# Kernel optimization log

Hardware: AMD Instinct MI355X
Metric: run time of the kernel (lower is better)

## Reference

```python
import jax, jax.numpy as jnp
import numpy as np
from jax import lax

WL = 140      # window_length
OFC = 118     # ofc_channel = window_length - 21 - 1
TDN = 21      # TimeDelayNum (sliding time-delay count)
D_CM = 16     # cm_attn embed dim
N_BR = 4      # conv_eeg_audio_number
C_OUT = 10    # conv_output_channel
KS = 9        # conv kernel size

def _init(key, shape, fan_in):
    return jax.random.uniform(key, shape, jnp.float32, -1.0, 1.0) / np.sqrt(fan_in)

def setup_inputs():
    key = jax.random.key(0)
    ks = jax.random.split(key, 12)
    return {
        "x": jax.random.normal(ks[0], (1, 1, 18, WL), dtype=jnp.float32),
        "tdA_in_w": _init(ks[1], (3 * OFC, OFC), OFC),
        "tdA_in_b": jnp.zeros((3 * OFC,), jnp.float32),
        "tdA_out_w": _init(ks[2], (OFC, OFC), OFC),
        "tdA_out_b": jnp.zeros((OFC,), jnp.float32),
        "tdB_in_w": _init(ks[3], (3 * OFC, OFC), OFC),
        "tdB_in_b": jnp.zeros((3 * OFC,), jnp.float32),
        "tdB_out_w": _init(ks[4], (OFC, OFC), OFC),
        "tdB_out_b": jnp.zeros((OFC,), jnp.float32),
        "cm_in_w": _init(ks[5], (N_BR, 3 * D_CM, D_CM), D_CM),
        "cm_in_b": jnp.zeros((N_BR, 3 * D_CM), jnp.float32),
        "cm_out_w": _init(ks[6], (N_BR, D_CM, D_CM), D_CM),
        "cm_out_b": jnp.zeros((N_BR, D_CM), jnp.float32),
        "projA_w": _init(ks[7], (16, 1), 1),
        "projB_w": _init(ks[8], (16, 1), 1),
        "conv_w": _init(ks[9], (N_BR, C_OUT, 16, KS), 16 * KS),
        "conv_b": jnp.zeros((N_BR, C_OUT), jnp.float32),
        "fc1_w": _init(ks[10], (40, 40), 40),
        "fc1_b": jnp.zeros((40,), jnp.float32),
        "fc2_w": _init(ks[11], (2, 40), 40),
        "fc2_b": jnp.zeros((2,), jnp.float32),
    }

def _mha(q, k, v, in_w, in_b, out_w, out_b):
    # single-head attention; q: (Lq, d), k/v: (Lk, d) -> (Lq, d)
    d = q.shape[-1]
    wq, wk, wv = jnp.split(in_w, 3, axis=0)
    bq, bk, bv = jnp.split(in_b, 3)
    qp = (q @ wq.T + bq) * (1.0 / np.sqrt(d))
    kp = k @ wk.T + bk
    vp = v @ wv.T + bv
    attn = jax.nn.softmax(qp @ kp.T, axis=-1)
    return (attn @ vp) @ out_w.T + out_b

def _forward(x, tdA_in_w, tdA_in_b, tdA_out_w, tdA_out_b,
             tdB_in_w, tdB_in_b, tdB_out_w, tdB_out_b,
             cm_in_w, cm_in_b, cm_out_w, cm_out_b,
             projA_w, projB_w, conv_w, conv_b,
             fc1_w, fc1_b, fc2_w, fc2_b):
    sig = x[0, 0]                               # (18, 140)
    wavA_raw, eeg_raw, wavB_raw = sig[0], sig[1:17], sig[17]
    # ChannelWav: sliding time-delay unfold -> (TDN, OFC)
    idx = jnp.arange(TDN)[:, None] + jnp.arange(OFC)[None, :]
    kA = wavA_raw[idx]                          # (21, 118)
    kB = wavB_raw[idx]
    eeg = eeg_raw[:, WL - OFC:]                 # (16, 118)
    # time-delay attention (embed_dim = 118, seq = 16 eeg channels / 21 delays)
    attA = _mha(eeg, kA, kA, tdA_in_w, tdA_in_b, tdA_out_w, tdA_out_b)  # (16, 118)
    attB = _mha(eeg, kB, kB, tdB_in_w, tdB_in_b, tdB_out_w, tdB_out_b)
    # select_max: pick attention row with largest total correlation to eeg
    iA = jnp.argmax(jnp.sum(eeg @ attA.T, axis=1))
    iB = jnp.argmax(jnp.sum(eeg @ attB.T, axis=1))
    wA = projA_w @ attA[iA][None, :]            # 1x1 conv == outer product, (16, 118)
    wB = projB_w @ attB[iB][None, :]
    data = [wA, eeg, eeg, wB]
    kv = [eeg, wA, wB, eeg]
    feats = []
    for i in range(N_BR):                       # 4 structurally distinct branches
        o = _mha(data[i].T, kv[i].T, kv[i].T,
                 cm_in_w[i], cm_in_b[i], cm_out_w[i], cm_out_b[i])      # (118, 16)
        y = lax.conv_general_dilated(o.T[None], conv_w[i], (1,), 'VALID')  # (1, 10, 110)
        y = jax.nn.relu(y[0] + conv_b[i][:, None])
        feats.append(jnp.max(y, axis=-1))       # AdaptiveMaxPool1d(1) -> (10,)
    flat = jnp.concatenate(feats)               # (40,)
    h = jax.nn.sigmoid(flat @ fc1_w.T + fc1_b)
    out = jax.nn.sigmoid(h @ fc2_w.T + fc2_b)
    return out[None, :]                         # (1, 2)

def reference(x, tdA_in_w, tdA_in_b, tdA_out_w, tdA_out_b,
              tdB_in_w, tdB_in_b, tdB_out_w, tdB_out_b,
              cm_in_w, cm_in_b, cm_out_w, cm_out_b,
              projA_w, projB_w, conv_w, conv_b,
              fc1_w, fc1_b, fc2_w, fc2_b):
    return _forward(x, tdA_in_w, tdA_in_b, tdA_out_w, tdA_out_b,
                    tdB_in_w, tdB_in_b, tdB_out_w, tdB_out_b,
                    cm_in_w, cm_in_b, cm_out_w, cm_out_b,
                    projA_w, projB_w, conv_w, conv_b,
                    fc1_w, fc1_b, fc2_w, fc2_b)
```

## Files before the change

kernel.cpp:

```cpp
#include <hip/hip_runtime.h>
#include <math.h>

#define WL   140
#define OFC  118
#define TDN  21
#define COUT 10
#define KS   9
#define IW_SZ (OFC * OFC)

#define PROJ_STRIDE 6848
#define KP_OFF      1888
#define VP_OFF      4368
#define WS_ATT_A    13696
#define WS_ATT_B    13824
#define WS_FEATS    13952
#define WS_FLAGS    14080

#define MAGIC 0x1F2E3D4C
#define NSLOTS 34

struct Params {
    const float *x;
    const float *tdA_in_w, *tdA_in_b, *tdA_out_w, *tdA_out_b;
    const float *tdB_in_w, *tdB_in_b, *tdB_out_w, *tdB_out_b;
    const float *cm_in_w, *cm_in_b, *cm_out_w, *cm_out_b;
    const float *projA_w, *projB_w, *conv_w, *conv_b;
    const float *fc1_w, *fc1_b, *fc2_w, *fc2_b;
    float *fc_unused;
    float *ws, *out;
};

struct TdSm {
    float owpad[OFC][122];
    float qpp[16][122];
    float kpp[TDN][122];
    float vpp[TDN][122];
    float attn[16][22];
    float acs[22];
    float avcs[120];
    float colsum[120];
    float Ssum[16];
    float avsel[120];
    int   sel;
};

struct BrSm {
    float arow[120];
    float pv[16];
    float eeg_s[16][OFC];
    float w_inT[16][48];
    float b_in[48];
    float tv[3][16];
    float w_out[16][16];
    float b_out[16];
    float cw[COUT * 16 * KS];
    float cb[COUT];
    float kpS[OFC][17];
    float vpS[OFC][17];
    float u[120], v2[120];
    float part_m[4][128];
    float part_l[4][128];
    float part_acc[4][OFC][17];
    float o2[OFC][17];
    float qpS[OFC][17];
    float a_[120], dvec[120];
    float Avec[16], Bvec[16];
    float Gc[COUT][KS], cb2[COUT];
    float y[COUT][22];
};

struct HdSm { float f[64]; float h[64]; };

union alignas(16) Sm { TdSm t; BrSm b; HdSm h; };

__device__ inline float wred(float v) {
    #pragma unroll
    for (int off = 32; off; off >>= 1) v += __shfl_xor(v, off);
    return v;
}

__device__ inline void postM(int* f, int tid) {
    __syncthreads();
    if (tid == 0)
        __hip_atomic_store(f, MAGIC, __ATOMIC_RELEASE, __HIP_MEMORY_SCOPE_AGENT);
}

__device__ inline void waitM(int* base, int first, int n, int tid) {
    if (tid == 0) {
        for (int i = 0; i < n; ++i) {
            int* f = base + (first + i) * 16;
            while (__hip_atomic_load(f, __ATOMIC_RELAXED, __HIP_MEMORY_SCOPE_AGENT) != MAGIC)
                __builtin_amdgcn_s_sleep(1);
        }
        __builtin_amdgcn_fence(__ATOMIC_ACQUIRE, "agent");
    }
    __syncthreads();
}

__device__ void td_proj_direct(int side, int lw, int lane, const Params& p)
{
    int sec, o, r, R;
    if (lw < 30) {
        sec = 0; o = lw * 4 + (lane & 3); r = lane >> 2; R = 16;
    } else {
        sec = (lw < 70) ? 1 : 2;
        int base = (lw - (sec == 1 ? 30 : 70)) * 3;
        o = base + lane % 3; r = lane / 3; R = TDN;
    }
    if (o >= OFC || r >= R) return;

    const float* in_w = (side ? p.tdB_in_w : p.tdA_in_w) + sec * IW_SZ + o * OFC;
    const float  bias = (side ? p.tdB_in_b : p.tdA_in_b)[sec * OFC + o];
    const float2* w2  = (const float2*)in_w;
    float s0 = 0.f;

    if (sec == 0) {
        const float2* a = (const float2*)(p.x + (1 + r) * WL + (WL - OFC));
        #pragma unroll 4
        for (int j = 0; j < 59; ++j) {
            float2 u = a[j], w = w2[j];
            s0 += u.x * w.x + u.y * w.y;
        }
        s0 = (s0 + bias) * (1.0f / sqrtf(118.0f));
    } else {
        const float* wr = p.x + (side ? 17 * WL : 0) + r;
        #pragma unroll 4
        for (int j = 0; j < 59; ++j) {
            float2 w = w2[j];
            s0 += wr[2 * j] * w.x + wr[2 * j + 1] * w.y;
        }
        s0 += bias;
    }
    p.ws[side * PROJ_STRIDE
         + (sec == 0 ? 0 : (sec == 1 ? KP_OFF : VP_OFF))
         + r * OFC + o] = s0;
}

__device__ void td_phase2(int b, int tid, const Params& p, TdSm& s)
{
    const float* base  = p.ws + b * PROJ_STRIDE;
    const float* out_b = b ? p.tdB_out_b : p.tdA_out_b;
    const int wid = tid >> 6, lane = tid & 63;

    for (int e = tid; e < 16 * 59; e += 512) {
        int r = e / 59, j = e - r * 59;
        ((float2*)&s.qpp[r][0])[j] = ((const float2*)(base + r * OFC))[j];
    }
    for (int e = tid; e < TDN * 59; e += 512) {
        int t = e / 59, j = e - t * 59;
        ((float2*)&s.kpp[t][0])[j] = ((const float2*)(base + KP_OFF + t * OFC))[j];
        ((float2*)&s.vpp[t][0])[j] = ((const float2*)(base + VP_OFF + t * OFC))[j];
    }
    __syncthreads();

    if (tid < 16 * TDN) {
        int i = tid / TDN, t = tid - (tid / TDN) * TDN;
        const float2* q = (const float2*)&s.qpp[i][0];
        const float2* k = (const float2*)&s.kpp[t][0];
        float sc = 0.f;
        #pragma unroll 4
        for (int j = 0; j < 59; ++j) {
            float2 u = q[j], v = k[j];
            sc += u.x * v.x + u.y * v.y;
        }
        s.attn[i][t] = sc;
    }
    __syncthreads();

    if (tid < 16) {
        float m = s.attn[tid][0];
        for (int t = 1; t < TDN; ++t) m = fmaxf(m, s.attn[tid][t]);
        float l = 0.f;
        for (int t = 0; t < TDN; ++t) {
            float pp = __expf(s.attn[tid][t] - m);
            s.attn[tid][t] = pp;
            l += pp;
        }
        float inv = 1.f / l;
        for (int t = 0; t < TDN; ++t) s.attn[tid][t] *= inv;
    }
    __syncthreads();

    if (tid < TDN) {
        float a = 0.f;
        for (int i = 0; i < 16; ++i) a += s.attn[i][tid];
        s.acs[tid] = a;
    }
    __syncthreads();

    if (tid < OFC) {
        float a = 0.f;
        for (int t = 0; t < TDN; ++t) a += s.acs[t] * s.vpp[t][tid];
        s.avcs[tid] = a;
    }
    __syncthreads();

    if (tid < OFC) {
        const float2* a  = (const float2*)&s.avcs[0];
        const float2* w2 = (const float2*)&s.owpad[tid][0];
        float a0 = 0.f;
        #pragma unroll 4
        for (int j = 0; j < 59; ++j) {
            float2 u = a[j], v = w2[j];
            a0 += u.x * v.x + u.y * v.y;
        }
        s.colsum[tid] = a0 + 16.f * out_b[tid];
    }
    __syncthreads();

    for (int d = wid; d < 16; d += 8) {
        const float* er = p.x + (1 + d) * WL + (WL - OFC);
        int j0 = lane * 2;
        float sc = 0.f;
        if (j0 < OFC) {
            float2 ev = *(const float2*)(er + j0);
            float2 cv = *(const float2*)(&s.colsum[j0]);
            sc = ev.x * cv.x + ev.y * cv.y;
        }
        sc = wred(sc);
        if (lane == 0) s.Ssum[d] = sc;
    }
    __syncthreads();

    if (tid == 0) {
        int best = 0; float bv = s.Ssum[0];
        for (int i = 1; i < 16; ++i)
            if (s.Ssum[i] > bv) { bv = s.Ssum[i]; best = i; }
        s.sel = best;
    }
    __syncthreads();

    if (tid < OFC) {
        float a = 0.f;
        for (int t = 0; t < TDN; ++t) a += s.attn[s.sel][t] * s.vpp[t][tid];
        s.avsel[tid] = a;
    }
    __syncthreads();

    if (tid < OFC) {
        const float2* a  = (const float2*)&s.avsel[0];
        const float2* w2 = (const float2*)&s.owpad[tid][0];
        float a0 = 0.f;
        #pragma unroll 4
        for (int j = 0; j < 59; ++j) {
            float2 u = a[j], v = w2[j];
            a0 += u.x * v.x + u.y * v.y;
        }
        p.ws[(b ? WS_ATT_B : WS_ATT_A) + tid] = a0 + out_b[tid];
    }
}

__device__ void br_pre(int br, int tid, const Params& p, BrSm& s)
{
    const bool d_r1 = (br == 0 || br == 3);

    for (int e = tid; e < 16 * OFC; e += 512) {
        int r = e / OFC, c = e - (e / OFC) * OFC;
        s.eeg_s[r][c] = p.x[(1 + r) * WL + (WL - OFC) + c];
    }
    for (int e = tid; e < 768; e += 512) {
        int q = e / 16, r = e % 16;
        s.w_inT[r][q] = p.cm_in_w[br * 768 + e];
    }
    if (tid < 48) s.b_in[tid] = p.cm_in_b[br * 48 + tid];
    if (tid >= 64 && tid < 320) {
        int e = tid - 64;
        s.w_out[e >> 4][e & 15] = p.cm_out_w[br * 256 + e];
    }
    if (tid >= 384 && tid < 400) s.b_out[tid - 384] = p.cm_out_b[br * 16 + (tid - 384)];
    for (int e = tid; e < COUT * 16 * KS; e += 512) s.cw[e] = p.conv_w[br * 1440 + e];
    if (tid >= 400 && tid < 410) s.cb[tid - 400] = p.conv_b[br * COUT + (tid - 400)];
    {
        const float* pvg = (br < 2) ? p.projA_w : p.projB_w;
        if (tid >= 416 && tid < 432) s.pv[tid - 416] = pvg[tid - 416];
    }
    __syncthreads();

    if (tid < 48) {
        float a = 0.f;
        #pragma unroll
        for (int r = 0; r < 16; ++r) a += s.pv[r] * s.w_inT[r][tid];
        s.tv[tid / 16][tid % 16] = a;
    }
    __syncthreads();

    if (d_r1) {
        for (int e = tid; e < 2 * OFC * 16; e += 512) {
            int sec01 = e / (OFC * 16);
            int rem = e - sec01 * OFC * 16;
            int j = rem >> 4, o = rem & 15;
            float a = 0.f;
            #pragma unroll
            for (int r = 0; r < 16; ++r) a += s.eeg_s[r][j] * s.w_inT[r][(1 + sec01) * 16 + o];
            a += s.b_in[(1 + sec01) * 16 + o];
            (sec01 ? &s.vpS[0][0] : &s.kpS[0][0])[j * 17 + o] = a;
        }
        __syncthreads();
        if (tid < OFC) {
            float uu = 0.f, vv = 0.f;
            #pragma unroll
            for (int o = 0; o < 16; ++o) {
                float kv = s.kpS[tid][o];
                uu += s.tv[0][o] * kv;
                vv += s.b_in[o] * kv;
            }
            s.u[tid] = uu; s.v2[tid] = vv;
        }
    } else {
        for (int e = tid; e < OFC * 16; e += 512) {
            int j = e >> 4, o = e & 15;
            float a = 0.f;
            #pragma unroll
            for (int r = 0; r < 16; ++r) a += s.eeg_s[r][j] * s.w_inT[r][o];
            s.qpS[j][o] = (a + s.b_in[o]) * 0.25f;
        }
        __syncthreads();
        if (tid < OFC) {
            float a = 0.f;
            #pragma unroll
            for (int o = 0; o < 16; ++o) a += s.qpS[tid][o] * s.tv[1][o];
            s.a_[tid] = a;
        }
        if (tid >= 128 && tid < 144) {
            int c = tid - 128;
            float A = 0.f, B = 0.f;
            #pragma unroll
            for (int o = 0; o < 16; ++o) {
                A += s.tv[2][o] * s.w_out[c][o];
                B += s.b_in[32 + o] * s.w_out[c][o];
            }
            s.Avec[c] = A;
            s.Bvec[c] = B + s.b_out[c];
        }
        __syncthreads();
        if (tid < COUT * KS) {
            int c = tid / KS, k = tid - (tid / KS) * KS;
            float g = 0.f;
            #pragma unroll
            for (int m = 0; m < 16; ++m) g += s.Avec[m] * s.cw[(c * 16 + m) * KS + k];
            s.Gc[c][k] = g;
        }
        if (tid >= 128 && tid < 128 + COUT) {
            int c = tid - 128;
            float cc = s.cb[c];
            #pragma unroll
            for (int m = 0; m < 16; ++m) {
                float bsum = 0.f;
                #pragma unroll
                for (int k = 0; k < KS; ++k) bsum += s.cw[(c * 16 + m) * KS + k];
                cc += s.Bvec[m] * bsum;
            }
            s.cb2[c] = cc;
        }
    }
}

__device__ void br_main(int br, int tid, const Params& p, BrSm& s)
{
    const bool d_r1 = (br == 0 || br == 3);
    const float* ar = p.ws + ((br < 2) ? WS_ATT_A : WS_ATT_B);
    if (tid < OFC) s.arow[tid] = ar[tid];
    __syncthreads();

    if (d_r1) {
        const int g = tid >> 7, j = tid & 127;
        float acc[16];
        float m = -INFINITY, l = 0.f;
        #pragma unroll
        for (int r = 0; r < 16; ++r) acc[r] = 0.f;

        if (j < OFC) {
            const float aj = s.arow[j];
            const int t0 = (g * OFC) >> 2, t1 = ((g + 1) * OFC) >> 2;
            for (int t = t0; t < t1; ++t) {
                float sc = 0.25f * fmaf(aj, s.u[t], s.v2[t]);
                float mn = fmaxf(m, sc);
                float c  = __expf(m - mn);
                float pp = __expf(sc - mn);
                l = l * c + pp;
                const float* vr = &s.vpS[t][0];
                #pragma unroll
                for (int r = 0; r < 16; ++r) acc[r] = acc[r] * c + pp * vr[r];
                m = mn;
            }
            s.part_m[g][j] = m;
            s.part_l[g][j] = l;
            #pragma unroll
            for (int r = 0; r < 16; ++r) s.part_acc[g][j][r] = acc[r];
        }
        __syncthreads();

        if (tid < OFC) {
            float m0 = s.part_m[0][tid], m1 = s.part_m[1][tid];
            float m2 = s.part_m[2][tid], m3 = s.part_m[3][tid];
            float mm = fmaxf(fmaxf(m0, m1), fmaxf(m2, m3));
            float c0 = __expf(m0 - mm), c1 = __expf(m1 - mm);
            float c2 = __expf(m2 - mm), c3 = __expf(m3 - mm);
            float ll = c0 * s.part_l[0][tid] + c1 * s.part_l[1][tid]
                     + c2 * s.part_l[2][tid] + c3 * s.part_l[3][tid];
            float inv = 1.f / ll;
            float orow[16];
            #pragma unroll
            for (int r = 0; r < 16; ++r)
                orow[r] = (c0 * s.part_acc[0][tid][r] + c1 * s.part_acc[1][tid][r]
                         + c2 * s.part_acc[2][tid][r] + c3 * s.part_acc[3][tid][r]) * inv;
            for (int c = 0; c < 16; ++c) {
                float a = s.b_out[c];
                #pragma unroll
                for (int d = 0; d < 16; ++d) a += orow[d] * s.w_out[c][d];
                s.o2[tid][c] = a;
            }
        }
        __syncthreads();

        if (tid < COUT * 22) {
            int c = tid / 22, grp = tid - (tid / 22) * 22;
            int pbase = grp * 5;
            float acc5[5];
            #pragma unroll
            for (int i = 0; i < 5; ++i) acc5[i] = s.cb[c];
            for (int mI = 0; mI < 16; ++mI) {
                float win[13];
                #pragma unroll
                for (int t = 0; t < 13; ++t) win[t] = s.o2[pbase + t][mI];
                #pragma unroll
                for (int k = 0; k < KS; ++k) {
                    float wv = s.cw[(c * 16 + mI) * KS + k];
                    #pragma unroll
                    for (int i = 0; i < 5; ++i) acc5[i] += win[i + k] * wv;
                }
            }
            float mx = fmaxf(fmaxf(fmaxf(acc5[0], acc5[1]), fmaxf(acc5[2], acc5[3])), acc5[4]);
            s.y[c][grp] = fmaxf(mx, 0.f);
        }
        __syncthreads();
    } else {
        if (tid < OFC) {
            const float aj = s.a_[tid];
            float m = -INFINITY;
            for (int t = 0; t < OFC; ++t) m = fmaxf(m, aj * s.arow[t]);
            float l = 0.f, d = 0.f;
            for (int t = 0; t < OFC; ++t) {
                float e = __expf(aj * s.arow[t] - m);
                l += e;
                d += e * s.arow[t];
            }
            s.dvec[tid] = d / l;
        }
        __syncthreads();

        if (tid < COUT * 22) {
            int c = tid / 22, grp = tid - (tid / 22) * 22;
            int pbase = grp * 5;
            float win[13];
            #pragma unroll
            for (int t = 0; t < 13; ++t) win[t] = s.dvec[pbase + t];
            float acc5[5];
            #pragma unroll
            for (int i = 0; i < 5; ++i) acc5[i] = s.cb2[c];
            #pragma unroll
            for (int k = 0; k < KS; ++k) {
                float wv = s.Gc[c][k];
                #pragma unroll
                for (int i = 0; i < 5; ++i) acc5[i] += win[i + k] * wv;
            }
            float mx = fmaxf(fmaxf(fmaxf(acc5[0], acc5[1]), fmaxf(acc5[2], acc5[3])), acc5[4]);
            s.y[c][grp] = fmaxf(mx, 0.f);
        }
        __syncthreads();
    }

    if (tid < COUT) {
        float mx = s.y[tid][0];
        for (int g2 = 1; g2 < 22; ++g2) mx = fmaxf(mx, s.y[tid][g2]);
        p.ws[WS_FEATS + br * COUT + tid] = mx;
    }
}

__global__ __launch_bounds__(512) void fused_net(Params p)
{
    __shared__ Sm sm;
    const int blk = blockIdx.x;
    const int tid = threadIdx.x;
    int* flags = (int*)(p.ws + WS_FLAGS);

    if (blk >= 2 && blk < 30) {
        const int side = (blk < 16) ? 0 : 1;
        const int gw   = (blk - (side ? 16 : 2)) * 8 + (tid >> 6);
        if (gw < 110) td_proj_direct(side, gw, tid & 63, p);
        postM(&flags[(blk - 2) * 16], tid);
        return;
    }

    if (blk < 2) {
        const float* ow = blk ? p.tdB_out_w : p.tdA_out_w;
        for (int e = tid; e < OFC * 59; e += 512) {
            int o = e / 59, j = e - o * 59;
            ((float2*)&sm.t.owpad[o][0])[j] = ((const float2*)(ow + o * OFC))[j];
        }
        waitM(flags, blk ? 14 : 0, 14, tid);
        td_phase2(blk, tid, p, sm.t);
        postM(&flags[(28 + blk) * 16], tid);

        if (blk == 0) {
            waitM(flags, 30, 4, tid);
            if (tid < NSLOTS)
                __hip_atomic_store(&flags[tid * 16], 0,
                                   __ATOMIC_RELAXED, __HIP_MEMORY_SCOPE_AGENT);
            __syncthreads();
            if (tid < 40) sm.h.f[tid] = p.ws[WS_FEATS + tid];
            __syncthreads();
            if (tid < 40) {
                float a = p.fc1_b[tid];
                for (int k = 0; k < 40; ++k) a += sm.h.f[k] * p.fc1_w[tid * 40 + k];
                sm.h.h[tid] = 1.f / (1.f + __expf(-a));
            }
            __syncthreads();
            if (tid < 2) {
                float a = p.fc2_b[tid];
                for (int k = 0; k < 40; ++k) a += sm.h.h[k] * p.fc2_w[tid * 40 + k];
                p.out[tid] = 1.f / (1.f + __expf(-a));
            }
        }
        return;
    }

    const int br = blk - 30;
    br_pre(br, tid, p, sm.b);
    waitM(flags, (br < 2) ? 28 : 29, 1, tid);
    br_main(br, tid, p, sm.b);
    postM(&flags[(30 + br) * 16], tid);
}

extern "C" void kernel_launch(void* const* d_in, const int* in_sizes, int n_in,
                              void* d_out, int out_size, void* d_ws, size_t ws_size,
                              hipStream_t stream) {
    Params prm;
    prm.x         = (const float*)d_in[0];
    prm.tdA_in_w  = (const float*)d_in[1];
    prm.tdA_in_b  = (const float*)d_in[2];
    prm.tdA_out_w = (const float*)d_in[3];
    prm.tdA_out_b = (const float*)d_in[4];
    prm.tdB_in_w  = (const float*)d_in[5];
    prm.tdB_in_b  = (const float*)d_in[6];
    prm.tdB_out_w = (const float*)d_in[7];
    prm.tdB_out_b = (const float*)d_in[8];
    prm.cm_in_w   = (const float*)d_in[9];
    prm.cm_in_b   = (const float*)d_in[10];
    prm.cm_out_w  = (const float*)d_in[11];
    prm.cm_out_b  = (const float*)d_in[12];
    prm.projA_w   = (const float*)d_in[13];
    prm.projB_w   = (const float*)d_in[14];
    prm.conv_w    = (const float*)d_in[15];
    prm.conv_b    = (const float*)d_in[16];
    prm.fc1_w     = (const float*)d_in[17];
    prm.fc1_b     = (const float*)d_in[18];
    prm.fc2_w     = (const float*)d_in[19];
    prm.fc2_b     = (const float*)d_in[20];
    prm.fc_unused = nullptr;
    prm.ws        = (float*)d_ws;
    prm.out       = (float*)d_out;

    fused_net<<<dim3(34), dim3(512), 0, stream>>>(prm);
}
```

Measured before the change: 39.75 us.

## Merge branch blocks into time-delay attention blocks to cut inter-block handoffs

Removes the four separate branch blocks. Each of the two time-delay attention blocks now computes its own two cross-modal branches (one query-side, one key-side) right after producing its attention row, keeping the row in shared memory instead of round-tripping through global workspace and flag waits. Branch preprocessing (weight staging, K/V projections, folded conv weights) is done before waiting on the projection blocks, so it overlaps with them. The final FC head runs in block 0 after a single flag from block 1. The cost is that each block does two branches serially, which lengthens the critical path, and it uses more shared memory.

```diff
diff --git a/kernel.cpp b/kernel.cpp
--- a/kernel.cpp
+++ b/kernel.cpp
@@ -11,13 +11,11 @@
 #define PROJ_STRIDE 6848
 #define KP_OFF      1888
 #define VP_OFF      4368
-#define WS_ATT_A    13696
-#define WS_ATT_B    13824
 #define WS_FEATS    13952
 #define WS_FLAGS    14080
 
-#define MAGIC 0x1F2E3D4C
-#define NSLOTS 34
+#define MAGIC  0x1F2E3D4C
+#define NSLOTS 29
 
 struct Params {
     const float *x;
@@ -26,17 +24,47 @@
     const float *cm_in_w, *cm_in_b, *cm_out_w, *cm_out_b;
     const float *projA_w, *projB_w, *conv_w, *conv_b;
     const float *fc1_w, *fc1_b, *fc2_w, *fc2_b;
-    float *fc_unused;
     float *ws, *out;
 };
 
-struct TdSm {
-    float owpad[OFC][122];
+struct PreScratch {
+    float w_inT[16][48];
+    float b_in[48];
+    float pv[16];
+    float kpS[OFC][17];
+    float qpS[OFC][17];
+    float tv[3][16];
+    float w_out_kr[16][16];
+    float b_out_kr[16];
+    float cw_kr[COUT * 16 * KS];
+    float cb_kr[16];
+    float Avec[16], Bvec[16];
+};
+
+struct QkvStage {
     float qpp[16][122];
     float kpp[TDN][122];
     float vpp[TDN][122];
+};
+
+struct Ph {
+    float owpad[OFC][122];
+    union { QkvStage qkv; PreScratch pre; } u2;
+};
+
+struct BrScratch {
+    float part_m[4][128];
+    float part_l[4][128];
+    float part_acc[4][OFC][17];
+    float o2[OFC][17];
+    float dvec[120];
+    float y[COUT][22];
+};
+
+struct MnSm {
+    union { Ph ph; BrScratch br; } u1;
     float attn[16][22];
-    float acs[22];
+    float acs[24];
     float avcs[120];
     float colsum[120];
     float Ssum[16];
@@ -44,34 +72,25 @@
     int   sel;
 };
 
-struct BrSm {
+struct Pers {
     float arow[120];
-    float pv[16];
-    float eeg_s[16][OFC];
-    float w_inT[16][48];
-    float b_in[48];
-    float tv[3][16];
-    float w_out[16][16];
-    float b_out[16];
-    float cw[COUT * 16 * KS];
-    float cb[COUT];
-    float kpS[OFC][17];
+    float eeg[16][120];
+    float bout[120];
+    float u[120], v2[120];
     float vpS[OFC][17];
-    float u[120], v2[120];
-    float part_m[4][128];
-    float part_l[4][128];
-    float part_acc[4][OFC][17];
-    float o2[OFC][17];
-    float qpS[OFC][17];
-    float a_[120], dvec[120];
-    float Avec[16], Bvec[16];
-    float Gc[COUT][KS], cb2[COUT];
-    float y[COUT][22];
-};
-
-struct HdSm { float f[64]; float h[64]; };
-
-union alignas(16) Sm { TdSm t; BrSm b; HdSm h; };
+    float w_out_dr[16][16];
+    float b_out_dr[16];
+    float cw_dr[COUT * 16 * KS];
+    float cb_dr[16];
+    float a_[120];
+    float Gc[COUT][KS];
+    float cb2[16];
+    float feats[40];
+    float fc1w[1600], fc1b[40], fc2w[80], fc2b[2];
+    float hh[40];
+};
+
+struct Sm { MnSm m; Pers p; };
 
 __device__ inline float wred(float v) {
     #pragma unroll
@@ -97,16 +116,12 @@
     __syncthreads();
 }
 
-__device__ void td_proj_direct(int side, int lw, int lane, const Params& p)
+__device__ void proj_task(int side, int lw, int lane, const Params& p)
 {
     int sec, o, r, R;
-    if (lw < 30) {
-        sec = 0; o = lw * 4 + (lane & 3); r = lane >> 2; R = 16;
-    } else {
-        sec = (lw < 70) ? 1 : 2;
-        int base = (lw - (sec == 1 ? 30 : 70)) * 3;
-        o = base + lane % 3; r = lane / 3; R = TDN;
-    }
+    if (lw < 30) { sec = 0; o = lw * 4 + (lane & 3); r = lane >> 2; R = 16; }
+    else if (lw < 70) { sec = 1; o = (lw - 30) * 3 + lane % 3; r = lane / 3; R = TDN; }
+    else { sec = 2; o = (lw - 70) * 3 + lane % 3; r = lane / 3; R = TDN; }
     if (o >= OFC || r >= R) return;
 
     const float* in_w = (side ? p.tdB_in_w : p.tdA_in_w) + sec * IW_SZ + o * OFC;
@@ -136,344 +151,393 @@
          + r * OFC + o] = s0;
 }
 
-__device__ void td_phase2(int b, int tid, const Params& p, TdSm& s)
+__device__ void main_block(int b, int tid, const Params& p, Sm& S)
 {
-    const float* base  = p.ws + b * PROJ_STRIDE;
-    const float* out_b = b ? p.tdB_out_b : p.tdA_out_b;
     const int wid = tid >> 6, lane = tid & 63;
-
+    int* flags = (int*)(p.ws + WS_FLAGS);
+    MnSm& m = S.m;
+    Pers& P = S.p;
+    const int dr = b ? 3 : 0;
+    const int kr = b ? 2 : 1;
+    const float* pvg = b ? p.projB_w : p.projA_w;
+    PreScratch& pr = m.u1.ph.u2.pre;
+
+    const float* ow = b ? p.tdB_out_w : p.tdA_out_w;
+    for (int e = tid; e < OFC * 59; e += 512) {
+        int o = e / 59, j = e - o * 59;
+        ((float2*)&m.u1.ph.owpad[o][0])[j] = ((const float2*)(ow + o * OFC))[j];
+    }
+    for (int e = tid; e < 16 * OFC; e += 512) {
+        int r = e / OFC, c = e - (e / OFC) * OFC;
+        P.eeg[r][c] = p.x[(1 + r) * WL + (WL - OFC) + c];
+    }
+    if (tid < OFC) P.bout[tid] = (b ? p.tdB_out_b : p.tdA_out_b)[tid];
+    for (int e = tid; e < 1440; e += 512) P.cw_dr[e] = p.conv_w[dr * 1440 + e];
+    if (tid < 256) P.w_out_dr[tid >> 4][tid & 15] = p.cm_out_w[dr * 256 + tid];
+    if (tid >= 256 && tid < 272) P.b_out_dr[tid - 256] = p.cm_out_b[dr * 16 + (tid - 256)];
+    if (tid >= 288 && tid < 288 + COUT) P.cb_dr[tid - 288] = p.conv_b[dr * COUT + (tid - 288)];
+    if (b == 0) {
+        for (int e = tid; e < 1600; e += 512) P.fc1w[e] = p.fc1_w[e];
+        if (tid < 40) P.fc1b[tid] = p.fc1_b[tid];
+        if (tid >= 320 && tid < 400) P.fc2w[tid - 320] = p.fc2_w[tid - 320];
+        if (tid >= 400 && tid < 402) P.fc2b[tid - 400] = p.fc2_b[tid - 400];
+    }
+    for (int e = tid; e < 768; e += 512) {
+        int q = e / 16, r = e % 16;
+        pr.w_inT[r][q] = p.cm_in_w[dr * 768 + e];
+    }
+    if (tid < 48) pr.b_in[tid] = p.cm_in_b[dr * 48 + tid];
+    if (tid >= 448 && tid < 464) pr.pv[tid - 448] = pvg[tid - 448];
+    __syncthreads();
+
+    if (tid < 16) {
+        float a = 0.f;
+        #pragma unroll
+        for (int r = 0; r < 16; ++r) a += pr.pv[r] * pr.w_inT[r][tid];
+        pr.tv[0][tid] = a;
+    }
+    __syncthreads();
+    for (int e = tid; e < 2 * OFC * 16; e += 512) {
+        int sec01 = e / (OFC * 16);
+        int rem = e - sec01 * OFC * 16;
+        int j = rem >> 4, o = rem & 15;
+        float a = 0.f;
+        #pragma unroll
+        for (int r = 0; r < 16; ++r) a += P.eeg[r][j] * pr.w_inT[r][(1 + sec01) * 16 + o];
+        a += pr.b_in[(1 + sec01) * 16 + o];
+        if (sec01) P.vpS[j][o] = a; else pr.kpS[j][o] = a;
+    }
+    __syncthreads();
+    if (tid < OFC) {
+        float uu = 0.f, vv = 0.f;
+        #pragma unroll
+        for (int o = 0; o < 16; ++o) {
+            float kv = pr.kpS[tid][o];
+            uu += pr.tv[0][o] * kv;
+            vv += pr.b_in[o] * kv;
+        }
+        P.u[tid] = uu; P.v2[tid] = vv;
+    }
+    __syncthreads();
+
+    for (int e = tid; e < 768; e += 512) {
+        int q = e / 16, r = e % 16;
+        pr.w_inT[r][q] = p.cm_in_w[kr * 768 + e];
+    }
+    if (tid < 48) pr.b_in[tid] = p.cm_in_b[kr * 48 + tid];
+    if (tid >= 64 && tid < 320) {
+        int e = tid - 64;
+        pr.w_out_kr[e >> 4][e & 15] = p.cm_out_w[kr * 256 + e];
+    }
+    if (tid >= 320 && tid < 336) pr.b_out_kr[tid - 320] = p.cm_out_b[kr * 16 + (tid - 320)];
+    for (int e = tid; e < 1440; e += 512) pr.cw_kr[e] = p.conv_w[kr * 1440 + e];
+    if (tid >= 336 && tid < 336 + COUT) pr.cb_kr[tid - 336] = p.conv_b[kr * COUT + (tid - 336)];
+    __syncthreads();
+    if (tid < 48) {
+        float a = 0.f;
+        #pragma unroll
+        for (int r = 0; r < 16; ++r) a += pr.pv[r] * pr.w_inT[r][tid];
+        pr.tv[tid / 16][tid % 16] = a;
+    }
+    __syncthreads();
+    for (int e = tid; e < OFC * 16; e += 512) {
+        int j = e >> 4, o = e & 15;
+        float a = 0.f;
+        #pragma unroll
+        for (int r = 0; r < 16; ++r) a += P.eeg[r][j] * pr.w_inT[r][o];
+        pr.qpS[j][o] = (a + pr.b_in[o]) * 0.25f;
+    }
+    __syncthreads();
+    if (tid < OFC) {
+        float a = 0.f;
+        #pragma unroll
+        for (int o = 0; o < 16; ++o) a += pr.qpS[tid][o] * pr.tv[1][o];
+        P.a_[tid] = a;
+    }
+    if (tid >= 128 && tid < 144) {
+        int c = tid - 128;
+        float A = 0.f, B = 0.f;
+        #pragma unroll
+        for (int o = 0; o < 16; ++o) {
+            A += pr.tv[2][o] * pr.w_out_kr[c][o];
+            B += pr.b_in[32 + o] * pr.w_out_kr[c][o];
+        }
+        pr.Avec[c] = A;
+        pr.Bvec[c] = B + pr.b_out_kr[c];
+    }
+    __syncthreads();
+    if (tid < COUT * KS) {
+        int c = tid / KS, k = tid - (tid / KS) * KS;
+        float g = 0.f;
+        #pragma unroll
+        for (int mm = 0; mm < 16; ++mm) g += pr.Avec[mm] * pr.cw_kr[(c * 16 + mm) * KS + k];
+        P.Gc[c][k] = g;
+    }
+    if (tid >= 128 && tid < 128 + COUT) {
+        int c = tid - 128;
+        float cc = pr.cb_kr[c];
+        #pragma unroll
+        for (int mm = 0; mm < 16; ++mm) {
+            float bs = 0.f;
+            #pragma unroll
+            for (int k = 0; k < KS; ++k) bs += pr.cw_kr[(c * 16 + mm) * KS + k];
+            cc += pr.Bvec[mm] * bs;
+        }
+        P.cb2[c] = cc;
+    }
+
+    waitM(flags, b * 14, 14, tid);
+    const float* base = p.ws + b * PROJ_STRIDE;
+    QkvStage& st = m.u1.ph.u2.qkv;
     for (int e = tid; e < 16 * 59; e += 512) {
         int r = e / 59, j = e - r * 59;
-        ((float2*)&s.qpp[r][0])[j] = ((const float2*)(base + r * OFC))[j];
+        ((float2*)&st.qpp[r][0])[j] = ((const float2*)(base + r * OFC))[j];
     }
     for (int e = tid; e < TDN * 59; e += 512) {
         int t = e / 59, j = e - t * 59;
-        ((float2*)&s.kpp[t][0])[j] = ((const float2*)(base + KP_OFF + t * OFC))[j];
-        ((float2*)&s.vpp[t][0])[j] = ((const float2*)(base + VP_OFF + t * OFC))[j];
+        ((float2*)&st.kpp[t][0])[j] = ((const float2*)(base + KP_OFF + t * OFC))[j];
+        ((float2*)&st.vpp[t][0])[j] = ((const float2*)(base + VP_OFF + t * OFC))[j];
     }
     __syncthreads();
 
     if (tid < 16 * TDN) {
         int i = tid / TDN, t = tid - (tid / TDN) * TDN;
-        const float2* q = (const float2*)&s.qpp[i][0];
-        const float2* k = (const float2*)&s.kpp[t][0];
+        const float2* q = (const float2*)&st.qpp[i][0];
+        const float2* k = (const float2*)&st.kpp[t][0];
         float sc = 0.f;
         #pragma unroll 4
         for (int j = 0; j < 59; ++j) {
             float2 u = q[j], v = k[j];
             sc += u.x * v.x + u.y * v.y;
         }
-        s.attn[i][t] = sc;
-    }
-    __syncthreads();
-
-    if (tid < 16) {
-        float m = s.attn[tid][0];
-        for (int t = 1; t < TDN; ++t) m = fmaxf(m, s.attn[tid][t]);
-        float l = 0.f;
-        for (int t = 0; t < TDN; ++t) {
-            float pp = __expf(s.attn[tid][t] - m);
-            s.attn[tid][t] = pp;
-            l += pp;
-        }
-        float inv = 1.f / l;
-        for (int t = 0; t < TDN; ++t) s.attn[tid][t] *= inv;
+        m.attn[i][t] = sc;
+    }
+    __syncthreads();
+
+    {
+        int row = wid * 2 + (lane >= 32 ? 1 : 0);
+        int t   = lane & 31;
+        float v = (t < TDN) ? m.attn[row][t] : -INFINITY;
+        float mx = v;
+        #pragma unroll
+        for (int off = 16; off; off >>= 1) mx = fmaxf(mx, __shfl_xor(mx, off, 32));
+        float pp = (t < TDN) ? __expf(v - mx) : 0.f;
+        float l = pp;
+        #pragma unroll
+        for (int off = 16; off; off >>= 1) l += __shfl_xor(l, off, 32);
+        if (t < TDN) m.attn[row][t] = pp / l;
     }
     __syncthreads();
 
     if (tid < TDN) {
         float a = 0.f;
-        for (int i = 0; i < 16; ++i) a += s.attn[i][tid];
-        s.acs[tid] = a;
-    }
-    __syncthreads();
-
-    if (tid < OFC) {
-        float a = 0.f;
-        for (int t = 0; t < TDN; ++t) a += s.acs[t] * s.vpp[t][tid];
-        s.avcs[tid] = a;
-    }
-    __syncthreads();
-
-    if (tid < OFC) {
-        const float2* a  = (const float2*)&s.avcs[0];
-        const float2* w2 = (const float2*)&s.owpad[tid][0];
+        for (int i = 0; i < 16; ++i) a += m.attn[i][tid];
+        m.acs[tid] = a;
+    }
+    __syncthreads();
+
+    if (tid < OFC) {
+        float a = 0.f;
+        #pragma unroll 3
+        for (int t = 0; t < TDN; ++t) a += m.acs[t] * st.vpp[t][tid];
+        m.avcs[tid] = a;
+    }
+    __syncthreads();
+
+    if (tid < OFC) {
+        const float2* a  = (const float2*)&m.avcs[0];
+        const float2* w2 = (const float2*)&m.u1.ph.owpad[tid][0];
         float a0 = 0.f;
         #pragma unroll 4
         for (int j = 0; j < 59; ++j) {
             float2 u = a[j], v = w2[j];
             a0 += u.x * v.x + u.y * v.y;
         }
-        s.colsum[tid] = a0 + 16.f * out_b[tid];
+        m.colsum[tid] = a0 + 16.f * P.bout[tid];
     }
     __syncthreads();
 
     for (int d = wid; d < 16; d += 8) {
-        const float* er = p.x + (1 + d) * WL + (WL - OFC);
         int j0 = lane * 2;
         float sc = 0.f;
         if (j0 < OFC) {
-            float2 ev = *(const float2*)(er + j0);
-            float2 cv = *(const float2*)(&s.colsum[j0]);
+            float2 ev = *(const float2*)(&P.eeg[d][j0]);
+            float2 cv = *(const float2*)(&m.colsum[j0]);
             sc = ev.x * cv.x + ev.y * cv.y;
         }
         sc = wred(sc);
-        if (lane == 0) s.Ssum[d] = sc;
+        if (lane == 0) m.Ssum[d] = sc;
     }
     __syncthreads();
 
     if (tid == 0) {
-        int best = 0; float bv = s.Ssum[0];
+        int best = 0; float bv = m.Ssum[0];
         for (int i = 1; i < 16; ++i)
-            if (s.Ssum[i] > bv) { bv = s.Ssum[i]; best = i; }
-        s.sel = best;
-    }
-    __syncthreads();
-
-    if (tid < OFC) {
-        float a = 0.f;
-        for (int t = 0; t < TDN; ++t) a += s.attn[s.sel][t] * s.vpp[t][tid];
-        s.avsel[tid] = a;
-    }
-    __syncthreads();
-
-    if (tid < OFC) {
-        const float2* a  = (const float2*)&s.avsel[0];
-        const float2* w2 = (const float2*)&s.owpad[tid][0];
+            if (m.Ssum[i] > bv) { bv = m.Ssum[i]; best = i; }
+        m.sel = best;
+    }
+    __syncthreads();
+
+    if (tid < OFC) {
+        float a = 0.f;
+        #pragma unroll 3
+        for (int t = 0; t < TDN; ++t) a += m.attn[m.sel][t] * st.vpp[t][tid];
+        m.avsel[tid] = a;
+    }
+    __syncthreads();
+
+    if (tid < OFC) {
+        const float2* a  = (const float2*)&m.avsel[0];
+        const float2* w2 = (const float2*)&m.u1.ph.owpad[tid][0];
         float a0 = 0.f;
         #pragma unroll 4
         for (int j = 0; j < 59; ++j) {
             float2 u = a[j], v = w2[j];
             a0 += u.x * v.x + u.y * v.y;
         }
-        p.ws[(b ? WS_ATT_B : WS_ATT_A) + tid] = a0 + out_b[tid];
-    }
-}
-
-__device__ void br_pre(int br, int tid, const Params& p, BrSm& s)
-{
-    const bool d_r1 = (br == 0 || br == 3);
-
-    for (int e = tid; e < 16 * OFC; e += 512) {
-        int r = e / OFC, c = e - (e / OFC) * OFC;
-        s.eeg_s[r][c] = p.x[(1 + r) * WL + (WL - OFC) + c];
-    }
-    for (int e = tid; e < 768; e += 512) {
-        int q = e / 16, r = e % 16;
-        s.w_inT[r][q] = p.cm_in_w[br * 768 + e];
-    }
-    if (tid < 48) s.b_in[tid] = p.cm_in_b[br * 48 + tid];
-    if (tid >= 64 && tid < 320) {
-        int e = tid - 64;
-        s.w_out[e >> 4][e & 15] = p.cm_out_w[br * 256 + e];
-    }
-    if (tid >= 384 && tid < 400) s.b_out[tid - 384] = p.cm_out_b[br * 16 + (tid - 384)];
-    for (int e = tid; e < COUT * 16 * KS; e += 512) s.cw[e] = p.conv_w[br * 1440 + e];
-    if (tid >= 400 && tid < 410) s.cb[tid - 400] = p.conv_b[br * COUT + (tid - 400)];
+        P.arow[tid] = a0 + P.bout[tid];
+    }
+    __syncthreads();
+
+    BrScratch& br = m.u1.br;
+
+    if (tid < OFC) {
+        const float aj = P.a_[tid];
+        float mx = -INFINITY;
+        for (int t = 0; t < OFC; ++t) mx = fmaxf(mx, aj * P.arow[t]);
+        float l = 0.f, d = 0.f;
+        for (int t = 0; t < OFC; ++t) {
+            float e = __expf(aj * P.arow[t] - mx);
+            l += e;
+            d += e * P.arow[t];
+        }
+        br.dvec[tid] = d / l;
+    }
+    __syncthreads();
+    if (tid < COUT * 22) {
+        int c = tid / 22, grp = tid - (tid / 22) * 22;
+        int pbase = grp * 5;
+        float win[13];
+        #pragma unroll
+        for (int t = 0; t < 13; ++t) win[t] = br.dvec[pbase + t];
+        float acc5[5];
+        #pragma unroll
+        for (int i = 0; i < 5; ++i) acc5[i] = P.cb2[c];
+        #pragma unroll
+        for (int k = 0; k < KS; ++k) {
+            float wv = P.Gc[c][k];
+            #pragma unroll
+            for (int i = 0; i < 5; ++i) acc5[i] += win[i + k] * wv;
+        }
+        float mx = fmaxf(fmaxf(fmaxf(acc5[0], acc5[1]), fmaxf(acc5[2], acc5[3])), acc5[4]);
+        br.y[c][grp] = fmaxf(mx, 0.f);
+    }
+    __syncthreads();
+    if (tid < COUT) {
+        float mx = br.y[tid][0];
+        for (int g2 = 1; g2 < 22; ++g2) mx = fmaxf(mx, br.y[tid][g2]);
+        P.feats[kr * COUT + tid] = mx;
+    }
+    __syncthreads();
+
     {
-        const float* pvg = (br < 2) ? p.projA_w : p.projB_w;
-        if (tid >= 416 && tid < 432) s.pv[tid - 416] = pvg[tid - 416];
-    }
-    __syncthreads();
-
-    if (tid < 48) {
-        float a = 0.f;
-        #pragma unroll
-        for (int r = 0; r < 16; ++r) a += s.pv[r] * s.w_inT[r][tid];
-        s.tv[tid / 16][tid % 16] = a;
-    }
-    __syncthreads();
-
-    if (d_r1) {
-        for (int e = tid; e < 2 * OFC * 16; e += 512) {
-            int sec01 = e / (OFC * 16);
-            int rem = e - sec01 * OFC * 16;
-            int j = rem >> 4, o = rem & 15;
-            float a = 0.f;
-            #pragma unroll
-            for (int r = 0; r < 16; ++r) a += s.eeg_s[r][j] * s.w_inT[r][(1 + sec01) * 16 + o];
-            a += s.b_in[(1 + sec01) * 16 + o];
-            (sec01 ? &s.vpS[0][0] : &s.kpS[0][0])[j * 17 + o] = a;
-        }
-        __syncthreads();
-        if (tid < OFC) {
-            float uu = 0.f, vv = 0.f;
-            #pragma unroll
-            for (int o = 0; o < 16; ++o) {
-                float kv = s.kpS[tid][o];
-                uu += s.tv[0][o] * kv;
-                vv += s.b_in[o] * kv;
-            }
-            s.u[tid] = uu; s.v2[tid] = vv;
-        }
-    } else {
-        for (int e = tid; e < OFC * 16; e += 512) {
-            int j = e >> 4, o = e & 15;
-            float a = 0.f;
-            #pragma unroll
-            for (int r = 0; r < 16; ++r) a += s.eeg_s[r][j] * s.w_inT[r][o];
-            s.qpS[j][o] = (a + s.b_in[o]) * 0.25f;
-        }
-        __syncthreads();
-        if (tid < OFC) {
-            float a = 0.f;
-            #pragma unroll
-            for (int o = 0; o < 16; ++o) a += s.qpS[tid][o] * s.tv[1][o];
-            s.a_[tid] = a;
-        }
-        if (tid >= 128 && tid < 144) {
-            int c = tid - 128;
-            float A = 0.f, B = 0.f;
-            #pragma unroll
-            for (int o = 0; o < 16; ++o) {
-                A += s.tv[2][o] * s.w_out[c][o];
-                B += s.b_in[32 + o] * s.w_out[c][o];
-            }
-            s.Avec[c] = A;
-            s.Bvec[c] = B + s.b_out[c];
-        }
-        __syncthreads();
-        if (tid < COUT * KS) {
-            int c = tid / KS, k = tid - (tid / KS) * KS;
-            float g = 0.f;
-            #pragma unroll
-            for (int m = 0; m < 16; ++m) g += s.Avec[m] * s.cw[(c * 16 + m) * KS + k];
-            s.Gc[c][k] = g;
-        }
-        if (tid >= 128 && tid < 128 + COUT) {
-            int c = tid - 128;
-            float cc = s.cb[c];
-            #pragma unroll
-            for (int m = 0; m < 16; ++m) {
-                float bsum = 0.f;
-                #pragma unroll
-                for (int k = 0; k < KS; ++k) bsum += s.cw[(c * 16 + m) * KS + k];
-                cc += s.Bvec[m] * bsum;
-            }
-            s.cb2[c] = cc;
-        }
-    }
-}
-
-__device__ void br_main(int br, int tid, const Params& p, BrSm& s)
-{
-    const bool d_r1 = (br == 0 || br == 3);
-    const float* ar = p.ws + ((br < 2) ? WS_ATT_A : WS_ATT_B);
-    if (tid < OFC) s.arow[tid] = ar[tid];
-    __syncthreads();
-
-    if (d_r1) {
         const int g = tid >> 7, j = tid & 127;
         float acc[16];
-        float m = -INFINITY, l = 0.f;
+        float mm = -INFINITY, l = 0.f;
         #pragma unroll
         for (int r = 0; r < 16; ++r) acc[r] = 0.f;
-
         if (j < OFC) {
-            const float aj = s.arow[j];
+            const float aj = P.arow[j];
             const int t0 = (g * OFC) >> 2, t1 = ((g + 1) * OFC) >> 2;
             for (int t = t0; t < t1; ++t) {
-                float sc = 0.25f * fmaf(aj, s.u[t], s.v2[t]);
-                float mn = fmaxf(m, sc);
-                float c  = __expf(m - mn);
+                float sc = 0.25f * fmaf(aj, P.u[t], P.v2[t]);
+                float mn = fmaxf(mm, sc);
+                float c  = __expf(mm - mn);
                 float pp = __expf(sc - mn);
                 l = l * c + pp;
-                const float* vr = &s.vpS[t][0];
+                const float* vr = &P.vpS[t][0];
                 #pragma unroll
                 for (int r = 0; r < 16; ++r) acc[r] = acc[r] * c + pp * vr[r];
-                m = mn;
+                mm = mn;
             }
-            s.part_m[g][j] = m;
-            s.part_l[g][j] = l;
+            br.part_m[g][j] = mm;
+            br.part_l[g][j] = l;
             #pragma unroll
-            for (int r = 0; r < 16; ++r) s.part_acc[g][j][r] = acc[r];
-        }
-        __syncthreads();
-
-        if (tid < OFC) {
-            float m0 = s.part_m[0][tid], m1 = s.part_m[1][tid];
-            float m2 = s.part_m[2][tid], m3 = s.part_m[3][tid];
-            float mm = fmaxf(fmaxf(m0, m1), fmaxf(m2, m3));
-            float c0 = __expf(m0 - mm), c1 = __expf(m1 - mm);
-            float c2 = __expf(m2 - mm), c3 = __expf(m3 - mm);
-            float ll = c0 * s.part_l[0][tid] + c1 * s.part_l[1][tid]
-                     + c2 * s.part_l[2][tid] + c3 * s.part_l[3][tid];
-            float inv = 1.f / ll;
-            float orow[16];
+            for (int r = 0; r < 16; ++r) br.part_acc[g][j][r] = acc[r];
+        }
+    }
+    __syncthreads();
+    if (tid < OFC) {
+        float m0 = br.part_m[0][tid], m1 = br.part_m[1][tid];
+        float m2 = br.part_m[2][tid], m3 = br.part_m[3][tid];
+        float mx = fmaxf(fmaxf(m0, m1), fmaxf(m2, m3));
+        float c0 = __expf(m0 - mx), c1 = __expf(m1 - mx);
+        float c2 = __expf(m2 - mx), c3 = __expf(m3 - mx);
+        float ll = c0 * br.part_l[0][tid] + c1 * br.part_l[1][tid]
+                 + c2 * br.part_l[2][tid] + c3 * br.part_l[3][tid];
+        float inv = 1.f / ll;
+        float orow[16];
+        #pragma unroll
+        for (int r = 0; r < 16; ++r)
+            orow[r] = (c0 * br.part_acc[0][tid][r] + c1 * br.part_acc[1][tid][r]
+                     + c2 * br.part_acc[2][tid][r] + c3 * br.part_acc[3][tid][r]) * inv;
+        for (int c = 0; c < 16; ++c) {
+            float a = P.b_out_dr[c];
             #pragma unroll
-            for (int r = 0; r < 16; ++r)
-                orow[r] = (c0 * s.part_acc[0][tid][r] + c1 * s.part_acc[1][tid][r]
-                         + c2 * s.part_acc[2][tid][r] + c3 * s.part_acc[3][tid][r]) * inv;
-            for (int c = 0; c < 16; ++c) {
-                float a = s.b_out[c];
-                #pragma unroll
-                for (int d = 0; d < 16; ++d) a += orow[d] * s.w_out[c][d];
-                s.o2[tid][c] = a;
-            }
-        }
-        __syncthreads();
-
-        if (tid < COUT * 22) {
-            int c = tid / 22, grp = tid - (tid / 22) * 22;
-            int pbase = grp * 5;
-            float acc5[5];
-            #pragma unroll
-            for (int i = 0; i < 5; ++i) acc5[i] = s.cb[c];
-            for (int mI = 0; mI < 16; ++mI) {
-                float win[13];
-                #pragma unroll
-                for (int t = 0; t < 13; ++t) win[t] = s.o2[pbase + t][mI];
-                #pragma unroll
-                for (int k = 0; k < KS; ++k) {
-                    float wv = s.cw[(c * 16 + mI) * KS + k];
-                    #pragma unroll
-                    for (int i = 0; i < 5; ++i) acc5[i] += win[i + k] * wv;
-                }
-            }
-            float mx = fmaxf(fmaxf(fmaxf(acc5[0], acc5[1]), fmaxf(acc5[2], acc5[3])), acc5[4]);
-            s.y[c][grp] = fmaxf(mx, 0.f);
-        }
-        __syncthreads();
-    } else {
-        if (tid < OFC) {
-            const float aj = s.a_[tid];
-            float m = -INFINITY;
-            for (int t = 0; t < OFC; ++t) m = fmaxf(m, aj * s.arow[t]);
-            float l = 0.f, d = 0.f;
-            for (int t = 0; t < OFC; ++t) {
-                float e = __expf(aj * s.arow[t] - m);
-                l += e;
-                d += e * s.arow[t];
-            }
-            s.dvec[tid] = d / l;
-        }
-        __syncthreads();
-
-        if (tid < COUT * 22) {
-            int c = tid / 22, grp = tid - (tid / 22) * 22;
-            int pbase = grp * 5;
+            for (int d = 0; d < 16; ++d) a += orow[d] * P.w_out_dr[c][d];
+            br.o2[tid][c] = a;
+        }
+    }
+    __syncthreads();
+    if (tid < COUT * 22) {
+        int c = tid / 22, grp = tid - (tid / 22) * 22;
+        int pbase = grp * 5;
+        float acc5[5];
+        #pragma unroll
+        for (int i = 0; i < 5; ++i) acc5[i] = P.cb_dr[c];
+        for (int mI = 0; mI < 16; ++mI) {
             float win[13];
             #pragma unroll
-            for (int t = 0; t < 13; ++t) win[t] = s.dvec[pbase + t];
-            float acc5[5];
-            #pragma unroll
-            for (int i = 0; i < 5; ++i) acc5[i] = s.cb2[c];
+            for (int t = 0; t < 13; ++t) win[t] = br.o2[pbase + t][mI];
             #pragma unroll
             for (int k = 0; k < KS; ++k) {
-                float wv = s.Gc[c][k];
+                float wv = P.cw_dr[(c * 16 + mI) * KS + k];
                 #pragma unroll
                 for (int i = 0; i < 5; ++i) acc5[i] += win[i + k] * wv;
             }
-            float mx = fmaxf(fmaxf(fmaxf(acc5[0], acc5[1]), fmaxf(acc5[2], acc5[3])), acc5[4]);
-            s.y[c][grp] = fmaxf(mx, 0.f);
-        }
+        }
+        float mx = fmaxf(fmaxf(fmaxf(acc5[0], acc5[1]), fmaxf(acc5[2], acc5[3])), acc5[4]);
+        br.y[c][grp] = fmaxf(mx, 0.f);
+    }
+    __syncthreads();
+    if (tid < COUT) {
+        float mx = br.y[tid][0];
+        for (int g2 = 1; g2 < 22; ++g2) mx = fmaxf(mx, br.y[tid][g2]);
+        P.feats[dr * COUT + tid] = mx;
+    }
+
+    if (b == 1) {
         __syncthreads();
-    }
-
-    if (tid < COUT) {
-        float mx = s.y[tid][0];
-        for (int g2 = 1; g2 < 22; ++g2) mx = fmaxf(mx, s.y[tid][g2]);
-        p.ws[WS_FEATS + br * COUT + tid] = mx;
+        if (tid < 20) p.ws[WS_FEATS + 20 + tid] = P.feats[20 + tid];
+        postM(&flags[28 * 16], tid);
+    } else {
+        waitM(flags, 28, 1, tid);
+        if (tid < NSLOTS)
+            __hip_atomic_store(&flags[tid * 16], 0,
+                               __ATOMIC_RELAXED, __HIP_MEMORY_SCOPE_AGENT);
+        if (tid < 20) P.feats[20 + tid] = p.ws[WS_FEATS + 20 + tid];
+        __syncthreads();
+        if (tid < 40) {
+            float a = P.fc1b[tid];
+            for (int k = 0; k < 40; ++k) a += P.feats[k] * P.fc1w[tid * 40 + k];
+            P.hh[tid] = 1.f / (1.f + __expf(-a));
+        }
+        __syncthreads();
+        if (tid < 2) {
+            float a = P.fc2b[tid];
+            for (int k = 0; k < 40; ++k) a += P.hh[k] * P.fc2w[tid * 40 + k];
+            p.out[tid] = 1.f / (1.f + __expf(-a));
+        }
     }
 }
 
@@ -484,52 +548,14 @@
     const int tid = threadIdx.x;
     int* flags = (int*)(p.ws + WS_FLAGS);
 
-    if (blk >= 2 && blk < 30) {
+    if (blk >= 2) {
         const int side = (blk < 16) ? 0 : 1;
         const int gw   = (blk - (side ? 16 : 2)) * 8 + (tid >> 6);
-        if (gw < 110) td_proj_direct(side, gw, tid & 63, p);
+        if (gw < 110) proj_task(side, gw, tid & 63, p);
         postM(&flags[(blk - 2) * 16], tid);
         return;
     }
-
-    if (blk < 2) {
-        const float* ow = blk ? p.tdB_out_w : p.tdA_out_w;
-        for (int e = tid; e < OFC * 59; e += 512) {
-            int o = e / 59, j = e - o * 59;
-            ((float2*)&sm.t.owpad[o][0])[j] = ((const float2*)(ow + o * OFC))[j];
-        }
-        waitM(flags, blk ? 14 : 0, 14, tid);
-        td_phase2(blk, tid, p, sm.t);
-        postM(&flags[(28 + blk) * 16], tid);
-
-        if (blk == 0) {
-            waitM(flags, 30, 4, tid);
-            if (tid < NSLOTS)
-                __hip_atomic_store(&flags[tid * 16], 0,
-                                   __ATOMIC_RELAXED, __HIP_MEMORY_SCOPE_AGENT);
-            __syncthreads();
-            if (tid < 40) sm.h.f[tid] = p.ws[WS_FEATS + tid];
-            __syncthreads();
-            if (tid < 40) {
-                float a = p.fc1_b[tid];
-                for (int k = 0; k < 40; ++k) a += sm.h.f[k] * p.fc1_w[tid * 40 + k];
-                sm.h.h[tid] = 1.f / (1.f + __expf(-a));
-            }
-            __syncthreads();
-            if (tid < 2) {
-                float a = p.fc2_b[tid];
-                for (int k = 0; k < 40; ++k) a += sm.h.h[k] * p.fc2_w[tid * 40 + k];
-                p.out[tid] = 1.f / (1.f + __expf(-a));
-            }
-        }
-        return;
-    }
-
-    const int br = blk - 30;
-    br_pre(br, tid, p, sm.b);
-    waitM(flags, (br < 2) ? 28 : 29, 1, tid);
-    br_main(br, tid, p, sm.b);
-    postM(&flags[(30 + br) * 16], tid);
+    main_block(blk, tid, p, sm);
 }
 
 extern "C" void kernel_launch(void* const* d_in, const int* in_sizes, int n_in,
@@ -557,9 +583,8 @@
     prm.fc1_b     = (const float*)d_in[18];
     prm.fc2_w     = (const float*)d_in[19];
     prm.fc2_b     = (const float*)d_in[20];
-    prm.fc_unused = nullptr;
     prm.ws        = (float*)d_ws;
     prm.out       = (float*)d_out;
 
-    fused_net<<<dim3(34), dim3(512), 0, stream>>>(prm);
-}
+    fused_net<<<dim3(30), dim3(512), 0, stream>>>(prm);
+}
```

Result: slower. 46.26 us (+16.4%).
